# Performance work log

Hardware: AMD Instinct MI355X
Metric: run time of the kernel (lower is better)

The kernel has to match this reference:

```python
import jax, jax.numpy as jnp
import numpy as np

B, T, IN, HID, HYP = 32, 1024, 512, 512, 256


def setup_inputs() -> dict:
    key = jax.random.key(0)
    ks = jax.random.split(key, 12)
    s = lambda *sh: 1.0 / np.sqrt(sh[-1])
    return {
        "x": jax.random.normal(ks[0], (B, T, IN), jnp.float32),
        "hidden": jax.random.normal(ks[1], (B, HID), jnp.float32),
        "W_start": jax.random.uniform(ks[2], (HYP, IN), jnp.float32, -s(HYP, IN), s(HYP, IN)),
        "b_start": jax.random.uniform(ks[3], (HYP,), jnp.float32, -s(HYP, IN), s(HYP, IN)),
        "W_mid": jax.random.uniform(ks[4], (HYP, HYP), jnp.float32, -s(HYP, HYP), s(HYP, HYP)),
        "b_mid": jax.random.uniform(ks[5], (HYP,), jnp.float32, -s(HYP, HYP), s(HYP, HYP)),
        "W_end": jax.random.uniform(ks[6], (HID, HYP), jnp.float32, -s(HID, HYP), s(HID, HYP)),
        "b_end": jax.random.uniform(ks[7], (HID,), jnp.float32, -s(HID, HYP), s(HID, HYP)),
        "W2": jax.random.uniform(ks[8], (HID, IN), jnp.float32, -s(HID, IN), s(HID, IN)),
        "b2": jax.random.uniform(ks[9], (HID,), jnp.float32, -s(HID, IN), s(HID, IN)),
    }


def _roll_sum_relu(b, hidden):
    # b: [B, T, H], hidden: [B, H]
    # recurrence: h_t = relu(roll(h_{t-1}, 1, axis=-1) + b_t)
    bt = jnp.swapaxes(b, 0, 1)  # [T, B, H]

    def step(h, b_t):
        h_new = jax.nn.relu(jnp.roll(h, 1, axis=-1) + b_t)
        return h_new, h_new

    _, outs = jax.lax.scan(step, hidden, bt)
    return jnp.swapaxes(outs, 0, 1)  # [B, T, H]


def reference(x, hidden, W_start, b_start, W_mid, b_mid, W_end, b_end, W2, b2):
    h = jax.nn.relu(jnp.einsum('bti,hi->bth', x, W_start) + b_start)
    h = jax.nn.relu(jnp.einsum('bth,gh->btg', h, W_mid) + b_mid)
    fc_end = jnp.einsum('btg,og->bto', h, W_end) + b_end
    sig = jax.nn.sigmoid(jnp.einsum('bti,oi->bto', x, W2) + b2)
    b = fc_end * sig  # [B, T, HID]
    outputs = _roll_sum_relu(b, hidden)
    return outputs, outputs[:, -1, :]
```

## Files before the change

### kernel.cpp

```cpp
#include <hip/hip_runtime.h>
#include <math.h>

#define B_   32
#define T_   1024
#define IN_  512
#define HID_ 512
#define HYP_ 256
#define M_   (B_ * T_)
#define R_   128
#define NSEG 8
#define SEGL 128
#define NCH  (B_ * HID_)

#define H1S  0
#define H2S  65536
#define STG  131072
#define LDS_BYTES 147456

typedef _Float16 half8_t __attribute__((ext_vector_type(8)));
typedef float    f32x4   __attribute__((ext_vector_type(4)));

typedef __attribute__((address_space(1))) const void* gptr_as1;
typedef __attribute__((address_space(3))) void*       lptr_as3;

__device__ __forceinline__ void gload_lds16(const void* g, void* l) {
    __builtin_amdgcn_global_load_lds((gptr_as1)g, (lptr_as3)l, 16, 0, 0);
}

#define VMCNT3() asm volatile("s_waitcnt vmcnt(3)" ::: "memory")
#define VMCNT2() asm volatile("s_waitcnt vmcnt(2)" ::: "memory")
#define VMCNT0() asm volatile("s_waitcnt vmcnt(0)" ::: "memory")
#define SBAR()   __builtin_amdgcn_s_barrier()
#define SCHED0() __builtin_amdgcn_sched_barrier(0)

__global__ __launch_bounds__(256) void cvt_all(
    const float* __restrict__ x,  _Float16* __restrict__ xh,
    const float* __restrict__ Ws, _Float16* __restrict__ wsh,
    const float* __restrict__ Wm, _Float16* __restrict__ wmh,
    const float* __restrict__ We, _Float16* __restrict__ weh,
    const float* __restrict__ W2, _Float16* __restrict__ w2h)
{
    const int blk = blockIdx.x;
    const float* src; _Float16* dst; int base;
    if      (blk < 8192) { src = x;  dst = xh;  base = blk; }
    else if (blk < 8256) { src = Ws; dst = wsh; base = blk - 8192; }
    else if (blk < 8288) { src = Wm; dst = wmh; base = blk - 8256; }
    else if (blk < 8352) { src = We; dst = weh; base = blk - 8288; }
    else                 { src = W2; dst = w2h; base = blk - 8352; }
    const int i = base * 2048 + threadIdx.x * 8;
    f32x4 v0 = *(const f32x4*)(src + i);
    f32x4 v1 = *(const f32x4*)(src + i + 4);
    half8_t h;
    h[0] = (_Float16)v0[0]; h[1] = (_Float16)v0[1];
    h[2] = (_Float16)v0[2]; h[3] = (_Float16)v0[3];
    h[4] = (_Float16)v1[0]; h[5] = (_Float16)v1[1];
    h[6] = (_Float16)v1[2]; h[7] = (_Float16)v1[3];
    *(half8_t*)(dst + i) = h;
}

__device__ __forceinline__ void stage512(const _Float16* src, int K,
                                         char* ldsbase, int tid)
{
#pragma unroll
    for (int q = 0; q < 2; ++q) {
        const int s = q * 512 + tid;
        const int g = s >> 6, c2 = (s >> 4) & 3, r = (s & 15) ^ c2;
        const char* gp = (const char*)src + (size_t)(g * 16 + r) * (K * 2) + c2 * 16;
        char* lp = ldsbase + (q * 512 + (tid & ~63)) * 16;
        gload_lds16(gp, lp);
    }
}

__device__ __forceinline__ void stageA(const _Float16* src, int K,
                                       char* ldsbase, int tid)
{
    const int s = tid;
    const int g = s >> 6, c2 = (s >> 4) & 3, r = (s & 15) ^ c2;
    const char* gp = (const char*)src + (size_t)(g * 16 + r) * (K * 2) + c2 * 16;
    char* lp = ldsbase + (tid & ~63) * 16;
    gload_lds16(gp, lp);
}

__device__ __forceinline__ void do_step16(const char* ab, const char* bb,
                                          int wm, int wn, int lsw,
                                          f32x4 acc[4][4])
{
    half8_t af[4], wf[4];
#pragma unroll
    for (int i = 0; i < 4; ++i)
        af[i] = *(const half8_t*)(ab + (wm * 4 + i) * 1024 + lsw);
#pragma unroll
    for (int j = 0; j < 4; ++j)
        wf[j] = *(const half8_t*)(bb + (wn * 4 + j) * 1024 + lsw);
#pragma unroll
    for (int i = 0; i < 4; ++i)
#pragma unroll
        for (int j = 0; j < 4; ++j)
            acc[i][j] = __builtin_amdgcn_mfma_f32_16x16x32_f16(af[i], wf[j], acc[i][j], 0, 0, 0);
}

__device__ __forceinline__ void epi_relu_lds(char* dst, const f32x4 acc[4][4],
                                             const float* __restrict__ bias,
                                             int wm, int wn, int lq, int lr)
{
#pragma unroll
    for (int j = 0; j < 4; ++j) {
        const int col = wn * 64 + j * 16 + lr;
        const float bv = bias[col];
        const int cc2 = (col & 31) >> 3;
        const int cpart = (col >> 5) * 8192 + cc2 * 256 + (col & 7) * 2;
#pragma unroll
        for (int i = 0; i < 4; ++i) {
#pragma unroll
            for (int rg = 0; rg < 4; ++rg) {
                const int row = wm * 64 + i * 16 + lq * 4 + rg;
                const float v = fmaxf(acc[i][j][rg] + bv, 0.f);
                *(_Float16*)(dst + cpart + (row >> 4) * 1024 +
                             (((row & 15) ^ cc2)) * 16) = (_Float16)v;
            }
        }
    }
}

__global__ __launch_bounds__(512, 2) void fused_mlp(
    const _Float16* __restrict__ xh,
    const _Float16* __restrict__ wsh, const float* __restrict__ bs,
    const _Float16* __restrict__ wmh, const float* __restrict__ bm,
    const _Float16* __restrict__ weh, const float* __restrict__ be,
    const _Float16* __restrict__ w2h, const float* __restrict__ b2,
    _Float16* __restrict__ bh)
{
    __shared__ __align__(16) char lds[LDS_BYTES];

    const int tid  = threadIdx.x;
    const int m0   = blockIdx.x * R_;
    const int lane = tid & 63;
    const int wave = tid >> 6;
    const int wm = wave >> 2;
    const int wn = wave & 3;
    const int lq = lane >> 4, lr = lane & 15;
    const int lsw = (lane ^ ((lane >> 4) & 3)) * 16;

    const _Float16* xrow = xh + (size_t)m0 * IN_;
    const f32x4 zero = {0.f, 0.f, 0.f, 0.f};

    {
        f32x4 acc[4][4];
#pragma unroll
        for (int i = 0; i < 4; ++i)
#pragma unroll
            for (int j = 0; j < 4; ++j) acc[i][j] = zero;

        stageA(xrow, IN_, lds + H2S, tid);
        stage512(wsh, IN_, lds + STG, tid);
        for (int s = 0; s < 15; ++s) {
            const int e = s + 1;
            stageA(xrow + e * 32, IN_, lds + H2S + (e & 1) * 8192, tid);
            stage512(wsh + e * 32, IN_, (e & 1) ? lds + H1S : lds + STG, tid);
            VMCNT3(); SCHED0(); SBAR(); SCHED0();
            const char* ab = lds + H2S + (s & 1) * 8192;
            const char* bb = (s & 1) ? lds + H1S : lds + STG;
            __builtin_amdgcn_s_setprio(1);
            do_step16(ab, bb, wm, wn, lsw, acc);
            __builtin_amdgcn_s_setprio(0);
            SCHED0(); SBAR(); SCHED0();
        }
        VMCNT0(); SCHED0(); SBAR(); SCHED0();
        do_step16(lds + H2S + 8192, lds + H1S, wm, wn, lsw, acc);
        __syncthreads();
        epi_relu_lds(lds + H1S, acc, bs, wm, wn, lq, lr);
        __syncthreads();
    }

    {
        f32x4 acc[4][4];
#pragma unroll
        for (int i = 0; i < 4; ++i)
#pragma unroll
            for (int j = 0; j < 4; ++j) acc[i][j] = zero;

        stage512(wmh, HYP_, lds + STG, tid);
        for (int s = 0; s < 7; ++s) {
            const int e = s + 1;
            stage512(wmh + e * 32, HYP_, (e & 1) ? lds + H2S : lds + STG, tid);
            VMCNT2(); SCHED0(); SBAR(); SCHED0();
            const char* ab = lds + H1S + s * 8192;
            const char* bb = (s & 1) ? lds + H2S : lds + STG;
            __builtin_amdgcn_s_setprio(1);
            do_step16(ab, bb, wm, wn, lsw, acc);
            __builtin_amdgcn_s_setprio(0);
            SCHED0(); SBAR(); SCHED0();
        }
        VMCNT0(); SCHED0(); SBAR(); SCHED0();
        do_step16(lds + H1S + 7 * 8192, lds + H2S, wm, wn, lsw, acc);
        __syncthreads();
        epi_relu_lds(lds + H2S, acc, bm, wm, wn, lq, lr);
        __syncthreads();
    }

#pragma unroll 1
    for (int half = 0; half < 2; ++half) {
        const int c0 = half * 256;
        const _Float16* wehh = weh + (size_t)c0 * HYP_;
        const _Float16* w2hh = w2h + (size_t)c0 * IN_;
        f32x4 accf[4][4], accs[4][4];
#pragma unroll
        for (int i = 0; i < 4; ++i)
#pragma unroll
            for (int j = 0; j < 4; ++j) { accf[i][j] = zero; accs[i][j] = zero; }

        stage512(wehh, HYP_, lds + STG, tid);
        for (int s = 0; s < 7; ++s) {
            const int e = s + 1;
            stage512(wehh + e * 32, HYP_, (e & 1) ? lds + H1S + 16384 : lds + STG, tid);
            VMCNT2(); SCHED0(); SBAR(); SCHED0();
            const char* ab = lds + H2S + s * 8192;
            const char* bb = (s & 1) ? lds + H1S + 16384 : lds + STG;
            __builtin_amdgcn_s_setprio(1);
            do_step16(ab, bb, wm, wn, lsw, accf);
            __builtin_amdgcn_s_setprio(0);
            SCHED0(); SBAR(); SCHED0();
        }
        {
            stageA(xrow, IN_, lds + H1S, tid);
            stage512(w2hh, IN_, lds + STG, tid);
            VMCNT3(); SCHED0(); SBAR(); SCHED0();
            __builtin_amdgcn_s_setprio(1);
            do_step16(lds + H2S + 7 * 8192, lds + H1S + 16384, wm, wn, lsw, accf);
            __builtin_amdgcn_s_setprio(0);
            SCHED0(); SBAR(); SCHED0();
        }
        for (int s = 8; s < 23; ++s) {
            const int e = s + 1, ts = e - 8;
            stageA(xrow + ts * 32, IN_, lds + H1S + (e & 1) * 8192, tid);
            stage512(w2hh + ts * 32, IN_, (e & 1) ? lds + H1S + 16384 : lds + STG, tid);
            VMCNT3(); SCHED0(); SBAR(); SCHED0();
            const char* ab = lds + H1S + (s & 1) * 8192;
            const char* bb = (s & 1) ? lds + H1S + 16384 : lds + STG;
            __builtin_amdgcn_s_setprio(1);
            do_step16(ab, bb, wm, wn, lsw, accs);
            __builtin_amdgcn_s_setprio(0);
            SCHED0(); SBAR(); SCHED0();
        }
        VMCNT0(); SCHED0(); SBAR(); SCHED0();
        do_step16(lds + H1S + 8192, lds + H1S + 16384, wm, wn, lsw, accs);
        __syncthreads();

#pragma unroll
        for (int j = 0; j < 4; ++j) {
            const int gcol = c0 + wn * 64 + j * 16 + lr;
            const float bev = be[gcol];
            const float b2v = b2[gcol];
#pragma unroll
            for (int i = 0; i < 4; ++i) {
#pragma unroll
                for (int rg = 0; rg < 4; ++rg) {
                    const int row = m0 + wm * 64 + i * 16 + lq * 4 + rg;
                    const float fc = accf[i][j][rg] + bev;
                    float sg = accs[i][j][rg] + b2v;
                    sg = 1.f / (1.f + __expf(-sg));
                    bh[(size_t)row * HID_ + gcol] = (_Float16)(fc * sg);
                }
            }
        }
        __syncthreads();
    }
}

__global__ __launch_bounds__(256) void seg_reduce(const _Float16* __restrict__ bh,
                                                  float* __restrict__ Sarr,
                                                  float* __restrict__ Darr)
{
    const int G = blockIdx.x * 256 + threadIdx.x;
    const int r = G & 511;
    const int seg = (G >> 9) & 7;
    const int b = G >> 12;
    const int chain = b * 512 + r;
    const _Float16* bb = bh + (size_t)b * (T_ * HID_);
    const int t0 = seg * SEGL;

    float S = 0.f, D = -__builtin_inff();
#pragma unroll 8
    for (int u = 0; u < SEGL; ++u) {
        const int t = t0 + u;
        const float v = (float)bb[t * 512 + ((r + t) & 511)];
        S += v;
        D = fmaxf(D + v, 0.f);
    }
    Sarr[seg * NCH + chain] = S;
    Darr[seg * NCH + chain] = D;
}

__global__ __launch_bounds__(64) void carry_scan(const float* __restrict__ hidden,
                                                 const float* __restrict__ Sarr,
                                                 const float* __restrict__ Darr,
                                                 float* __restrict__ carry,
                                                 float* __restrict__ hlast)
{
    const int chain = blockIdx.x * 64 + threadIdx.x;
    const int b = chain >> 9, r = chain & 511;
    float c = hidden[b * 512 + ((r + 511) & 511)];
#pragma unroll
    for (int j = 0; j < NSEG; ++j) {
        carry[j * NCH + chain] = c;
        c = fmaxf(c + Sarr[j * NCH + chain], Darr[j * NCH + chain]);
    }
    hlast[b * 512 + ((r + 1023) & 511)] = c;
}

__global__ __launch_bounds__(256) void seg_apply(const _Float16* __restrict__ bh,
                                                 const float* __restrict__ carry,
                                                 float* __restrict__ out)
{
    const int G = blockIdx.x * 256 + threadIdx.x;
    const int r = G & 511;
    const int seg = (G >> 9) & 7;
    const int b = G >> 12;
    const int chain = b * 512 + r;
    const _Float16* bb = bh + (size_t)b * (T_ * HID_);
    float* ob = out + (size_t)b * (T_ * HID_);
    const int t0 = seg * SEGL;

    float c = carry[seg * NCH + chain];
#pragma unroll 8
    for (int u = 0; u < SEGL; ++u) {
        const int t = t0 + u;
        const int idx = t * 512 + ((r + t) & 511);
        c = fmaxf(c + (float)bb[idx], 0.f);
        ob[idx] = c;
    }
}

extern "C" void kernel_launch(void* const* d_in, const int* in_sizes, int n_in,
                              void* d_out, int out_size, void* d_ws, size_t ws_size,
                              hipStream_t stream)
{
    const float* x      = (const float*)d_in[0];
    const float* hidden = (const float*)d_in[1];
    const float* Ws     = (const float*)d_in[2];
    const float* bs     = (const float*)d_in[3];
    const float* Wm     = (const float*)d_in[4];
    const float* bm     = (const float*)d_in[5];
    const float* We     = (const float*)d_in[6];
    const float* be     = (const float*)d_in[7];
    const float* W2     = (const float*)d_in[8];
    const float* b2     = (const float*)d_in[9];

    float* outputs = (float*)d_out;
    float* hlast   = outputs + (size_t)M_ * HID_;

    _Float16* xh = (_Float16*)d_out;

    _Float16* bh   = (_Float16*)d_ws;
    _Float16* wsh  = bh + (size_t)M_ * HID_;
    _Float16* wmh  = wsh + HYP_ * IN_;
    _Float16* weh  = wmh + HYP_ * HYP_;
    _Float16* w2h  = weh + HID_ * HYP_;
    float*    Sarr = (float*)(w2h + HID_ * IN_);
    float*    Darr = Sarr + NSEG * NCH;
    float*    carr = Darr + NSEG * NCH;

    cvt_all<<<dim3(8480), 256, 0, stream>>>(x, xh, Ws, wsh, Wm, wmh, We, weh, W2, w2h);
    fused_mlp<<<dim3(M_ / R_), 512, 0, stream>>>(
        xh, wsh, bs, wmh, bm, weh, be, w2h, b2, bh);
    seg_reduce<<<dim3((NCH * NSEG) / 256), 256, 0, stream>>>(bh, Sarr, Darr);
    carry_scan<<<dim3(NCH / 64), 64, 0, stream>>>(hidden, Sarr, Darr, carr, hlast);
    seg_apply<<<dim3((NCH * NSEG) / 256), 256, 0, stream>>>(bh, carr, outputs);
}
```

Before: 120.3 us.

## Double K-step to 64 per barrier and prefetch next GEMM weights across stages

Each pipeline stage now stages and consumes 64 K-elements instead of 32, which halves the number of barrier and waitcnt rounds in every GEMM loop. The first weight tile of each following GEMM is issued during the last step of the preceding one, so the load overlaps the tail compute and epilogue. LDS use grows to 160 KB and the buffer offsets are reassigned. This risks lower occupancy and LDS aliasing mistakes in the new layout.

```diff
diff --git a/kernel.cpp b/kernel.cpp
--- a/kernel.cpp
+++ b/kernel.cpp
@@ -15,7 +15,7 @@
 #define H1S  0
 #define H2S  65536
 #define STG  131072
-#define LDS_BYTES 147456
+#define LDS_BYTES 163840
 
 typedef _Float16 half8_t __attribute__((ext_vector_type(8)));
 typedef float    f32x4   __attribute__((ext_vector_type(4)));
@@ -27,8 +27,8 @@
     __builtin_amdgcn_global_load_lds((gptr_as1)g, (lptr_as3)l, 16, 0, 0);
 }
 
-#define VMCNT3() asm volatile("s_waitcnt vmcnt(3)" ::: "memory")
-#define VMCNT2() asm volatile("s_waitcnt vmcnt(2)" ::: "memory")
+#define VMCNT6() asm volatile("s_waitcnt vmcnt(6)" ::: "memory")
+#define VMCNT4() asm volatile("s_waitcnt vmcnt(4)" ::: "memory")
 #define VMCNT0() asm volatile("s_waitcnt vmcnt(0)" ::: "memory")
 #define SBAR()   __builtin_amdgcn_s_barrier()
 #define SCHED0() __builtin_amdgcn_sched_barrier(0)
@@ -81,6 +81,20 @@
     gload_lds16(gp, lp);
 }
 
+__device__ __forceinline__ void stageA64(const _Float16* src, int K,
+                                         char* ldsbase, int tid)
+{
+    stageA(src,      K, ldsbase,        tid);
+    stageA(src + 32, K, ldsbase + 8192, tid);
+}
+
+__device__ __forceinline__ void stageW64(const _Float16* src, int K,
+                                         char* ldsbase, int tid)
+{
+    stage512(src,      K, ldsbase,         tid);
+    stage512(src + 32, K, ldsbase + 16384, tid);
+}
+
 __device__ __forceinline__ void do_step16(const char* ab, const char* bb,
                                           int wm, int wn, int lsw,
                                           f32x4 acc[4][4])
@@ -97,6 +111,14 @@
 #pragma unroll
         for (int j = 0; j < 4; ++j)
             acc[i][j] = __builtin_amdgcn_mfma_f32_16x16x32_f16(af[i], wf[j], acc[i][j], 0, 0, 0);
+}
+
+__device__ __forceinline__ void do_step32(const char* ab, const char* bb,
+                                          int wm, int wn, int lsw,
+                                          f32x4 acc[4][4])
+{
+    do_step16(ab,        bb,         wm, wn, lsw, acc);
+    do_step16(ab + 8192, bb + 16384, wm, wn, lsw, acc);
 }
 
 __device__ __forceinline__ void epi_relu_lds(char* dst, const f32x4 acc[4][4],
@@ -151,22 +173,25 @@
 #pragma unroll
             for (int j = 0; j < 4; ++j) acc[i][j] = zero;
 
-        stageA(xrow, IN_, lds + H2S, tid);
-        stage512(wsh, IN_, lds + STG, tid);
-        for (int s = 0; s < 15; ++s) {
+        stageA64(xrow, IN_, lds + H2S, tid);
+        stageW64(wsh, IN_, lds + STG, tid);
+        for (int s = 0; s < 7; ++s) {
             const int e = s + 1;
-            stageA(xrow + e * 32, IN_, lds + H2S + (e & 1) * 8192, tid);
-            stage512(wsh + e * 32, IN_, (e & 1) ? lds + H1S : lds + STG, tid);
-            VMCNT3(); SCHED0(); SBAR(); SCHED0();
-            const char* ab = lds + H2S + (s & 1) * 8192;
-            const char* bb = (s & 1) ? lds + H1S : lds + STG;
+            stageA64(xrow + e * 64, IN_, lds + H2S + (e & 1) * 16384, tid);
+            stageW64(wsh + e * 64, IN_, (e & 1) ? lds + H2S + 32768 : lds + STG, tid);
+            VMCNT6(); SCHED0(); SBAR(); SCHED0();
+            const char* ab = lds + H2S + (s & 1) * 16384;
+            const char* bb = (s & 1) ? lds + H2S + 32768 : lds + STG;
             __builtin_amdgcn_s_setprio(1);
-            do_step16(ab, bb, wm, wn, lsw, acc);
+            do_step32(ab, bb, wm, wn, lsw, acc);
             __builtin_amdgcn_s_setprio(0);
             SCHED0(); SBAR(); SCHED0();
         }
-        VMCNT0(); SCHED0(); SBAR(); SCHED0();
-        do_step16(lds + H2S + 8192, lds + H1S, wm, wn, lsw, acc);
+        stageW64(wmh, HYP_, lds + STG, tid);
+        VMCNT4(); SCHED0(); SBAR(); SCHED0();
+        __builtin_amdgcn_s_setprio(1);
+        do_step32(lds + H2S + 16384, lds + H2S + 32768, wm, wn, lsw, acc);
+        __builtin_amdgcn_s_setprio(0);
         __syncthreads();
         epi_relu_lds(lds + H1S, acc, bs, wm, wn, lq, lr);
         __syncthreads();
@@ -179,20 +204,22 @@
 #pragma unroll
             for (int j = 0; j < 4; ++j) acc[i][j] = zero;
 
-        stage512(wmh, HYP_, lds + STG, tid);
-        for (int s = 0; s < 7; ++s) {
+        for (int s = 0; s < 3; ++s) {
             const int e = s + 1;
-            stage512(wmh + e * 32, HYP_, (e & 1) ? lds + H2S : lds + STG, tid);
-            VMCNT2(); SCHED0(); SBAR(); SCHED0();
-            const char* ab = lds + H1S + s * 8192;
+            stageW64(wmh + e * 64, HYP_, (e & 1) ? lds + H2S : lds + STG, tid);
+            VMCNT4(); SCHED0(); SBAR(); SCHED0();
+            const char* ab = lds + H1S + s * 16384;
             const char* bb = (s & 1) ? lds + H2S : lds + STG;
             __builtin_amdgcn_s_setprio(1);
-            do_step16(ab, bb, wm, wn, lsw, acc);
+            do_step32(ab, bb, wm, wn, lsw, acc);
             __builtin_amdgcn_s_setprio(0);
             SCHED0(); SBAR(); SCHED0();
         }
-        VMCNT0(); SCHED0(); SBAR(); SCHED0();
-        do_step16(lds + H1S + 7 * 8192, lds + H2S, wm, wn, lsw, acc);
+        stageW64(weh, HYP_, lds + STG, tid);
+        VMCNT4(); SCHED0(); SBAR(); SCHED0();
+        __builtin_amdgcn_s_setprio(1);
+        do_step32(lds + H1S + 49152, lds + H2S, wm, wn, lsw, acc);
+        __builtin_amdgcn_s_setprio(0);
         __syncthreads();
         epi_relu_lds(lds + H2S, acc, bm, wm, wn, lq, lr);
         __syncthreads();
@@ -209,41 +236,47 @@
 #pragma unroll
             for (int j = 0; j < 4; ++j) { accf[i][j] = zero; accs[i][j] = zero; }
 
-        stage512(wehh, HYP_, lds + STG, tid);
+        for (int s = 0; s < 3; ++s) {
+            const int e = s + 1;
+            stageW64(wehh + e * 64, HYP_, (e & 1) ? lds + H1S : lds + STG, tid);
+            VMCNT4(); SCHED0(); SBAR(); SCHED0();
+            const char* ab = lds + H2S + s * 16384;
+            const char* bb = (s & 1) ? lds + H1S : lds + STG;
+            __builtin_amdgcn_s_setprio(1);
+            do_step32(ab, bb, wm, wn, lsw, accf);
+            __builtin_amdgcn_s_setprio(0);
+            SCHED0(); SBAR(); SCHED0();
+        }
+        stageA64(xrow, IN_, lds + H1S + 32768, tid);
+        stageW64(w2hh, IN_, lds + STG, tid);
+        VMCNT6(); SCHED0(); SBAR(); SCHED0();
+        __builtin_amdgcn_s_setprio(1);
+        do_step32(lds + H2S + 49152, lds + H1S, wm, wn, lsw, accf);
+        __builtin_amdgcn_s_setprio(0);
+        SCHED0(); SBAR(); SCHED0();
+
         for (int s = 0; s < 7; ++s) {
             const int e = s + 1;
-            stage512(wehh + e * 32, HYP_, (e & 1) ? lds + H1S + 16384 : lds + STG, tid);
-            VMCNT2(); SCHED0(); SBAR(); SCHED0();
-            const char* ab = lds + H2S + s * 8192;
-            const char* bb = (s & 1) ? lds + H1S + 16384 : lds + STG;
+            stageA64(xrow + e * 64, IN_, lds + H1S + 32768 + (e & 1) * 16384, tid);
+            stageW64(w2hh + e * 64, IN_, (e & 1) ? lds + H1S : lds + STG, tid);
+            VMCNT6(); SCHED0(); SBAR(); SCHED0();
+            const char* ab = lds + H1S + 32768 + (s & 1) * 16384;
+            const char* bb = (s & 1) ? lds + H1S : lds + STG;
             __builtin_amdgcn_s_setprio(1);
-            do_step16(ab, bb, wm, wn, lsw, accf);
+            do_step32(ab, bb, wm, wn, lsw, accs);
             __builtin_amdgcn_s_setprio(0);
             SCHED0(); SBAR(); SCHED0();
         }
-        {
-            stageA(xrow, IN_, lds + H1S, tid);
-            stage512(w2hh, IN_, lds + STG, tid);
-            VMCNT3(); SCHED0(); SBAR(); SCHED0();
-            __builtin_amdgcn_s_setprio(1);
-            do_step16(lds + H2S + 7 * 8192, lds + H1S + 16384, wm, wn, lsw, accf);
-            __builtin_amdgcn_s_setprio(0);
-            SCHED0(); SBAR(); SCHED0();
-        }
-        for (int s = 8; s < 23; ++s) {
-            const int e = s + 1, ts = e - 8;
-            stageA(xrow + ts * 32, IN_, lds + H1S + (e & 1) * 8192, tid);
-            stage512(w2hh + ts * 32, IN_, (e & 1) ? lds + H1S + 16384 : lds + STG, tid);
-            VMCNT3(); SCHED0(); SBAR(); SCHED0();
-            const char* ab = lds + H1S + (s & 1) * 8192;
-            const char* bb = (s & 1) ? lds + H1S + 16384 : lds + STG;
-            __builtin_amdgcn_s_setprio(1);
-            do_step16(ab, bb, wm, wn, lsw, accs);
-            __builtin_amdgcn_s_setprio(0);
-            SCHED0(); SBAR(); SCHED0();
-        }
-        VMCNT0(); SCHED0(); SBAR(); SCHED0();
-        do_step16(lds + H1S + 8192, lds + H1S + 16384, wm, wn, lsw, accs);
+        if (half == 0) {
+            stageW64(weh + (size_t)256 * HYP_, HYP_, lds + STG, tid);
+            VMCNT4();
+        } else {
+            VMCNT0();
+        }
+        SCHED0(); SBAR(); SCHED0();
+        __builtin_amdgcn_s_setprio(1);
+        do_step32(lds + H1S + 49152, lds + H1S, wm, wn, lsw, accs);
+        __builtin_amdgcn_s_setprio(0);
         __syncthreads();
 
 #pragma unroll
```

After: 117.7 us. -2.1%, faster.

## Load fp32 x directly into LDS, drop x conversion pass, halve row tile

Applied to the files above, without the earlier changes.

Removes the separate pass that converted x to fp16. The MLP kernel now stages fp32 x straight into LDS and converts it to fp16 in registers before each MFMA. The row tile drops from 128 to 64 so LDS use falls enough for four blocks per CU, and the next stage's weights are prefetched during each stage's final step. The cost is twice the fp32 A-tile bytes moved, extra conversion instructions, and weights re-read by twice as many blocks.

```diff
diff --git a/kernel.cpp b/kernel.cpp
--- a/kernel.cpp
+++ b/kernel.cpp
@@ -7,15 +7,15 @@
 #define HID_ 512
 #define HYP_ 256
 #define M_   (B_ * T_)
-#define R_   128
+#define R_   64
 #define NSEG 8
 #define SEGL 128
 #define NCH  (B_ * HID_)
 
 #define H1S  0
-#define H2S  65536
-#define STG  131072
-#define LDS_BYTES 147456
+#define H2S  32768
+#define STG  65536
+#define LDS_BYTES 81920
 
 typedef _Float16 half8_t __attribute__((ext_vector_type(8)));
 typedef float    f32x4   __attribute__((ext_vector_type(4)));
@@ -33,8 +33,7 @@
 #define SBAR()   __builtin_amdgcn_s_barrier()
 #define SCHED0() __builtin_amdgcn_sched_barrier(0)
 
-__global__ __launch_bounds__(256) void cvt_all(
-    const float* __restrict__ x,  _Float16* __restrict__ xh,
+__global__ __launch_bounds__(256) void cvt_w(
     const float* __restrict__ Ws, _Float16* __restrict__ wsh,
     const float* __restrict__ Wm, _Float16* __restrict__ wmh,
     const float* __restrict__ We, _Float16* __restrict__ weh,
@@ -42,11 +41,10 @@
 {
     const int blk = blockIdx.x;
     const float* src; _Float16* dst; int base;
-    if      (blk < 8192) { src = x;  dst = xh;  base = blk; }
-    else if (blk < 8256) { src = Ws; dst = wsh; base = blk - 8192; }
-    else if (blk < 8288) { src = Wm; dst = wmh; base = blk - 8256; }
-    else if (blk < 8352) { src = We; dst = weh; base = blk - 8288; }
-    else                 { src = W2; dst = w2h; base = blk - 8352; }
+    if      (blk < 64)  { src = Ws; dst = wsh; base = blk; }
+    else if (blk < 96)  { src = Wm; dst = wmh; base = blk - 64; }
+    else if (blk < 160) { src = We; dst = weh; base = blk - 96; }
+    else                { src = W2; dst = w2h; base = blk - 160; }
     const int i = base * 2048 + threadIdx.x * 8;
     f32x4 v0 = *(const f32x4*)(src + i);
     f32x4 v1 = *(const f32x4*)(src + i + 4);
@@ -71,35 +69,60 @@
     }
 }
 
-__device__ __forceinline__ void stageA(const _Float16* src, int K,
-                                       char* ldsbase, int tid)
-{
-    const int s = tid;
+__device__ __forceinline__ void stageA32(const float* src, int K,
+                                         char* ldsbase, int tid)
+{
+    const int p = tid >> 8;
+    const int s = tid & 255;
     const int g = s >> 6, c2 = (s >> 4) & 3, r = (s & 15) ^ c2;
-    const char* gp = (const char*)src + (size_t)(g * 16 + r) * (K * 2) + c2 * 16;
-    char* lp = ldsbase + (tid & ~63) * 16;
+    const char* gp = (const char*)(src + (size_t)(g * 16 + r) * K + c2 * 8 + p * 4);
+    char* lp = ldsbase + p * 4096 + (s & ~63) * 16;
     gload_lds16(gp, lp);
 }
 
-__device__ __forceinline__ void do_step16(const char* ab, const char* bb,
-                                          int wm, int wn, int lsw,
-                                          f32x4 acc[4][4])
-{
-    half8_t af[4], wf[4];
-#pragma unroll
-    for (int i = 0; i < 4; ++i)
-        af[i] = *(const half8_t*)(ab + (wm * 4 + i) * 1024 + lsw);
-#pragma unroll
-    for (int j = 0; j < 4; ++j)
-        wf[j] = *(const half8_t*)(bb + (wn * 4 + j) * 1024 + lsw);
-#pragma unroll
-    for (int i = 0; i < 4; ++i)
-#pragma unroll
-        for (int j = 0; j < 4; ++j)
-            acc[i][j] = __builtin_amdgcn_mfma_f32_16x16x32_f16(af[i], wf[j], acc[i][j], 0, 0, 0);
-}
-
-__device__ __forceinline__ void epi_relu_lds(char* dst, const f32x4 acc[4][4],
+__device__ __forceinline__ half8_t cvt8(f32x4 a, f32x4 b)
+{
+    half8_t h;
+    h[0] = (_Float16)a[0]; h[1] = (_Float16)a[1];
+    h[2] = (_Float16)a[2]; h[3] = (_Float16)a[3];
+    h[4] = (_Float16)b[0]; h[5] = (_Float16)b[1];
+    h[6] = (_Float16)b[2]; h[7] = (_Float16)b[3];
+    return h;
+}
+
+__device__ __forceinline__ void do_step8(const char* ab, const char* bb,
+                                         int wm, int wn, int lsw,
+                                         f32x4 acc[2][4])
+{
+    half8_t a0 = *(const half8_t*)(ab + (wm * 2 + 0) * 1024 + lsw);
+    half8_t a1 = *(const half8_t*)(ab + (wm * 2 + 1) * 1024 + lsw);
+#pragma unroll
+    for (int j = 0; j < 4; ++j) {
+        half8_t wf = *(const half8_t*)(bb + (wn * 4 + j) * 1024 + lsw);
+        acc[0][j] = __builtin_amdgcn_mfma_f32_16x16x32_f16(a0, wf, acc[0][j], 0, 0, 0);
+        acc[1][j] = __builtin_amdgcn_mfma_f32_16x16x32_f16(a1, wf, acc[1][j], 0, 0, 0);
+    }
+}
+
+__device__ __forceinline__ void do_step8_fa(const char* ab, const char* bb,
+                                            int wm, int wn, int lsw,
+                                            f32x4 acc[2][4])
+{
+    f32x4 p00 = *(const f32x4*)(ab + (wm * 2 + 0) * 1024 + lsw);
+    f32x4 p01 = *(const f32x4*)(ab + 4096 + (wm * 2 + 0) * 1024 + lsw);
+    f32x4 p10 = *(const f32x4*)(ab + (wm * 2 + 1) * 1024 + lsw);
+    f32x4 p11 = *(const f32x4*)(ab + 4096 + (wm * 2 + 1) * 1024 + lsw);
+    half8_t a0 = cvt8(p00, p01);
+    half8_t a1 = cvt8(p10, p11);
+#pragma unroll
+    for (int j = 0; j < 4; ++j) {
+        half8_t wf = *(const half8_t*)(bb + (wn * 4 + j) * 1024 + lsw);
+        acc[0][j] = __builtin_amdgcn_mfma_f32_16x16x32_f16(a0, wf, acc[0][j], 0, 0, 0);
+        acc[1][j] = __builtin_amdgcn_mfma_f32_16x16x32_f16(a1, wf, acc[1][j], 0, 0, 0);
+    }
+}
+
+__device__ __forceinline__ void epi_relu_lds(char* dst, const f32x4 acc[2][4],
                                              const float* __restrict__ bias,
                                              int wm, int wn, int lq, int lr)
 {
@@ -108,12 +131,12 @@
         const int col = wn * 64 + j * 16 + lr;
         const float bv = bias[col];
         const int cc2 = (col & 31) >> 3;
-        const int cpart = (col >> 5) * 8192 + cc2 * 256 + (col & 7) * 2;
-#pragma unroll
-        for (int i = 0; i < 4; ++i) {
+        const int cpart = (col >> 5) * 4096 + cc2 * 256 + (col & 7) * 2;
+#pragma unroll
+        for (int i = 0; i < 2; ++i) {
 #pragma unroll
             for (int rg = 0; rg < 4; ++rg) {
-                const int row = wm * 64 + i * 16 + lq * 4 + rg;
+                const int row = wm * 32 + i * 16 + lq * 4 + rg;
                 const float v = fmaxf(acc[i][j][rg] + bv, 0.f);
                 *(_Float16*)(dst + cpart + (row >> 4) * 1024 +
                              (((row & 15) ^ cc2)) * 16) = (_Float16)v;
@@ -122,8 +145,8 @@
     }
 }
 
-__global__ __launch_bounds__(512, 2) void fused_mlp(
-    const _Float16* __restrict__ xh,
+__global__ __launch_bounds__(512, 4) void fused_mlp(
+    const float* __restrict__ x,
     const _Float16* __restrict__ wsh, const float* __restrict__ bs,
     const _Float16* __restrict__ wmh, const float* __restrict__ bm,
     const _Float16* __restrict__ weh, const float* __restrict__ be,
@@ -141,58 +164,65 @@
     const int lq = lane >> 4, lr = lane & 15;
     const int lsw = (lane ^ ((lane >> 4) & 3)) * 16;
 
-    const _Float16* xrow = xh + (size_t)m0 * IN_;
+    const float* xrow = x + (size_t)m0 * IN_;
     const f32x4 zero = {0.f, 0.f, 0.f, 0.f};
 
     {
-        f32x4 acc[4][4];
-#pragma unroll
-        for (int i = 0; i < 4; ++i)
+        f32x4 acc[2][4];
+#pragma unroll
+        for (int i = 0; i < 2; ++i)
 #pragma unroll
             for (int j = 0; j < 4; ++j) acc[i][j] = zero;
 
-        stageA(xrow, IN_, lds + H2S, tid);
+        stageA32(xrow, IN_, lds + H2S + 16384, tid);
         stage512(wsh, IN_, lds + STG, tid);
+        __syncthreads();
+
         for (int s = 0; s < 15; ++s) {
             const int e = s + 1;
-            stageA(xrow + e * 32, IN_, lds + H2S + (e & 1) * 8192, tid);
-            stage512(wsh + e * 32, IN_, (e & 1) ? lds + H1S : lds + STG, tid);
-            VMCNT3(); SCHED0(); SBAR(); SCHED0();
-            const char* ab = lds + H2S + (s & 1) * 8192;
-            const char* bb = (s & 1) ? lds + H1S : lds + STG;
+            stageA32(xrow + e * 32, IN_, lds + H2S + 16384 + (e & 1) * 8192, tid);
+            stage512(wsh + e * 32, IN_, (e & 1) ? lds + H2S : lds + STG, tid);
+            SCHED0(); VMCNT3(); SCHED0(); SBAR(); SCHED0();
+            const char* ab = lds + H2S + 16384 + (s & 1) * 8192;
+            const char* bb = (s & 1) ? lds + H2S : lds + STG;
             __builtin_amdgcn_s_setprio(1);
-            do_step16(ab, bb, wm, wn, lsw, acc);
+            do_step8_fa(ab, bb, wm, wn, lsw, acc);
             __builtin_amdgcn_s_setprio(0);
             SCHED0(); SBAR(); SCHED0();
         }
-        VMCNT0(); SCHED0(); SBAR(); SCHED0();
-        do_step16(lds + H2S + 8192, lds + H1S, wm, wn, lsw, acc);
+        stage512(wmh, HYP_, lds + STG, tid);
+        SCHED0(); VMCNT2(); SCHED0(); SBAR(); SCHED0();
+        __builtin_amdgcn_s_setprio(1);
+        do_step8_fa(lds + H2S + 16384 + 8192, lds + H2S, wm, wn, lsw, acc);
+        __builtin_amdgcn_s_setprio(0);
         __syncthreads();
         epi_relu_lds(lds + H1S, acc, bs, wm, wn, lq, lr);
         __syncthreads();
     }
 
     {
-        f32x4 acc[4][4];
-#pragma unroll
-        for (int i = 0; i < 4; ++i)
+        f32x4 acc[2][4];
+#pragma unroll
+        for (int i = 0; i < 2; ++i)
 #pragma unroll
             for (int j = 0; j < 4; ++j) acc[i][j] = zero;
 
-        stage512(wmh, HYP_, lds + STG, tid);
         for (int s = 0; s < 7; ++s) {
             const int e = s + 1;
             stage512(wmh + e * 32, HYP_, (e & 1) ? lds + H2S : lds + STG, tid);
-            VMCNT2(); SCHED0(); SBAR(); SCHED0();
-            const char* ab = lds + H1S + s * 8192;
+            SCHED0(); VMCNT2(); SCHED0(); SBAR(); SCHED0();
+            const char* ab = lds + H1S + s * 4096;
             const char* bb = (s & 1) ? lds + H2S : lds + STG;
             __builtin_amdgcn_s_setprio(1);
-            do_step16(ab, bb, wm, wn, lsw, acc);
+            do_step8(ab, bb, wm, wn, lsw, acc);
             __builtin_amdgcn_s_setprio(0);
             SCHED0(); SBAR(); SCHED0();
         }
-        VMCNT0(); SCHED0(); SBAR(); SCHED0();
-        do_step16(lds + H1S + 7 * 8192, lds + H2S, wm, wn, lsw, acc);
+        stage512(weh, HYP_, lds + STG, tid);
+        SCHED0(); VMCNT2(); SCHED0(); SBAR(); SCHED0();
+        __builtin_amdgcn_s_setprio(1);
+        do_step8(lds + H1S + 7 * 4096, lds + H2S, wm, wn, lsw, acc);
+        __builtin_amdgcn_s_setprio(0);
         __syncthreads();
         epi_relu_lds(lds + H2S, acc, bm, wm, wn, lq, lr);
         __syncthreads();
@@ -203,47 +233,54 @@
         const int c0 = half * 256;
         const _Float16* wehh = weh + (size_t)c0 * HYP_;
         const _Float16* w2hh = w2h + (size_t)c0 * IN_;
-        f32x4 accf[4][4], accs[4][4];
-#pragma unroll
-        for (int i = 0; i < 4; ++i)
+        f32x4 accf[2][4], accs[2][4];
+#pragma unroll
+        for (int i = 0; i < 2; ++i)
 #pragma unroll
             for (int j = 0; j < 4; ++j) { accf[i][j] = zero; accs[i][j] = zero; }
 
-        stage512(wehh, HYP_, lds + STG, tid);
         for (int s = 0; s < 7; ++s) {
             const int e = s + 1;
-            stage512(wehh + e * 32, HYP_, (e & 1) ? lds + H1S + 16384 : lds + STG, tid);
-            VMCNT2(); SCHED0(); SBAR(); SCHED0();
-            const char* ab = lds + H2S + s * 8192;
-            const char* bb = (s & 1) ? lds + H1S + 16384 : lds + STG;
+            stage512(wehh + e * 32, HYP_, (e & 1) ? lds + H1S : lds + STG, tid);
+            SCHED0(); VMCNT2(); SCHED0(); SBAR(); SCHED0();
+            const char* ab = lds + H2S + s * 4096;
+            const char* bb = (s & 1) ? lds + H1S : lds + STG;
             __builtin_amdgcn_s_setprio(1);
-            do_step16(ab, bb, wm, wn, lsw, accf);
+            do_step8(ab, bb, wm, wn, lsw, accf);
             __builtin_amdgcn_s_setprio(0);
             SCHED0(); SBAR(); SCHED0();
         }
         {
-            stageA(xrow, IN_, lds + H1S, tid);
+            stageA32(xrow, IN_, lds + H1S + 16384, tid);
             stage512(w2hh, IN_, lds + STG, tid);
-            VMCNT3(); SCHED0(); SBAR(); SCHED0();
+            SCHED0(); VMCNT3(); SCHED0(); SBAR(); SCHED0();
             __builtin_amdgcn_s_setprio(1);
-            do_step16(lds + H2S + 7 * 8192, lds + H1S + 16384, wm, wn, lsw, accf);
+            do_step8(lds + H2S + 7 * 4096, lds + H1S, wm, wn, lsw, accf);
             __builtin_amdgcn_s_setprio(0);
             SCHED0(); SBAR(); SCHED0();
         }
-        for (int s = 8; s < 23; ++s) {
-            const int e = s + 1, ts = e - 8;
-            stageA(xrow + ts * 32, IN_, lds + H1S + (e & 1) * 8192, tid);
-            stage512(w2hh + ts * 32, IN_, (e & 1) ? lds + H1S + 16384 : lds + STG, tid);
-            VMCNT3(); SCHED0(); SBAR(); SCHED0();
-            const char* ab = lds + H1S + (s & 1) * 8192;
-            const char* bb = (s & 1) ? lds + H1S + 16384 : lds + STG;
+        for (int s = 0; s < 15; ++s) {
+            const int e = s + 1;
+            stageA32(xrow + e * 32, IN_, lds + H1S + 16384 + (e & 1) * 8192, tid);
+            stage512(w2hh + e * 32, IN_, (e & 1) ? lds + H1S : lds + STG, tid);
+            SCHED0(); VMCNT3(); SCHED0(); SBAR(); SCHED0();
+            const char* ab = lds + H1S + 16384 + (s & 1) * 8192;
+            const char* bb = (s & 1) ? lds + H1S : lds + STG;
             __builtin_amdgcn_s_setprio(1);
-            do_step16(ab, bb, wm, wn, lsw, accs);
+            do_step8_fa(ab, bb, wm, wn, lsw, accs);
             __builtin_amdgcn_s_setprio(0);
             SCHED0(); SBAR(); SCHED0();
         }
-        VMCNT0(); SCHED0(); SBAR(); SCHED0();
-        do_step16(lds + H1S + 8192, lds + H1S + 16384, wm, wn, lsw, accs);
+        if (half == 0) {
+            stage512(weh + (size_t)256 * HYP_, HYP_, lds + STG, tid);
+            SCHED0(); VMCNT2();
+        } else {
+            VMCNT0();
+        }
+        SCHED0(); SBAR(); SCHED0();
+        __builtin_amdgcn_s_setprio(1);
+        do_step8_fa(lds + H1S + 16384 + 8192, lds + H1S, wm, wn, lsw, accs);
+        __builtin_amdgcn_s_setprio(0);
         __syncthreads();
 
 #pragma unroll
@@ -252,10 +289,10 @@
             const float bev = be[gcol];
             const float b2v = b2[gcol];
 #pragma unroll
-            for (int i = 0; i < 4; ++i) {
+            for (int i = 0; i < 2; ++i) {
 #pragma unroll
                 for (int rg = 0; rg < 4; ++rg) {
-                    const int row = m0 + wm * 64 + i * 16 + lq * 4 + rg;
+                    const int row = m0 + wm * 32 + i * 16 + lq * 4 + rg;
                     const float fc = accf[i][j][rg] + bev;
                     float sg = accs[i][j][rg] + b2v;
                     sg = 1.f / (1.f + __expf(-sg));
@@ -349,8 +386,6 @@
     float* outputs = (float*)d_out;
     float* hlast   = outputs + (size_t)M_ * HID_;
 
-    _Float16* xh = (_Float16*)d_out;
-
     _Float16* bh   = (_Float16*)d_ws;
     _Float16* wsh  = bh + (size_t)M_ * HID_;
     _Float16* wmh  = wsh + HYP_ * IN_;
@@ -360,9 +395,9 @@
     float*    Darr = Sarr + NSEG * NCH;
     float*    carr = Darr + NSEG * NCH;
 
-    cvt_all<<<dim3(8480), 256, 0, stream>>>(x, xh, Ws, wsh, Wm, wmh, We, weh, W2, w2h);
+    cvt_w<<<dim3(288), 256, 0, stream>>>(Ws, wsh, Wm, wmh, We, weh, W2, w2h);
     fused_mlp<<<dim3(M_ / R_), 512, 0, stream>>>(
-        xh, wsh, bs, wmh, bm, weh, be, w2h, b2, bh);
+        x, wsh, bs, wmh, bm, weh, be, w2h, b2, bh);
     seg_reduce<<<dim3((NCH * NSEG) / 256), 256, 0, stream>>>(bh, Sarr, Darr);
     carry_scan<<<dim3(NCH / 64), 64, 0, stream>>>(hidden, Sarr, Darr, carr, hlast);
     seg_apply<<<dim3((NCH * NSEG) / 256), 256, 0, stream>>>(bh, carr, outputs);
```

Result: slower. 139.7 us (+16.1%).
